# Kernel tuning notes

Measured on AMD Instinct MI355X. Metric: run time of the kernel, lower is better.

## Reference

```python
import jax, jax.numpy as jnp
import numpy as np
import math

B, H, W, Cv, Ct, T = 8, 64, 64, 256, 512, 100
TOP_M = 5
N_PAD = 8  # last N_PAD text tokens are all-zero padding


def _xavier(key, fi, fo):
    lim = math.sqrt(6.0 / (fi + fo))
    return jax.random.uniform(key, (fi, fo), jnp.float32, -lim, lim)


def layernorm(x, g, b, eps=1e-5):
    m = x.mean(-1, keepdims=True)
    v = ((x - m) ** 2).mean(-1, keepdims=True)
    return (x - m) * jax.lax.rsqrt(v + eps) * g + b


def l2norm(x, eps=1e-6):
    n = jnp.sqrt((x * x).sum(-1, keepdims=True))
    return x / jnp.maximum(n, eps)


def setup_inputs() -> dict:
    key = jax.random.key(0)
    ks = jax.random.split(key, 10)
    visual = jax.random.normal(ks[0], (B, H, W, Cv), jnp.float32)
    text = jax.random.normal(ks[1], (B, T, Ct), jnp.float32)
    text = text.at[:, T - N_PAD:, :].set(0.0)  # padded tokens
    return {
        'visual_features': visual,
        'text_features': text,
        'ln1_g': jnp.ones((Cv,), jnp.float32),
        'ln1_b': jnp.zeros((Cv,), jnp.float32),
        'qw': _xavier(ks[2], Cv, Ct), 'qb': jnp.zeros((Ct,), jnp.float32),
        'vw': _xavier(ks[3], Ct, Cv), 'vb': jnp.zeros((Cv,), jnp.float32),
        'gate_w': jax.random.normal(ks[4], (Cv, 1), jnp.float32) * 0.02,
        'gate_b': jnp.zeros((1,), jnp.float32),
        'logit_scale': jnp.asarray(math.log(1.0 / 0.07), jnp.float32),
        'alpha': jnp.asarray(0.1, jnp.float32),
        'ln2_g': jnp.ones((Cv,), jnp.float32),
        'ln2_b': jnp.zeros((Cv,), jnp.float32),
        'w1': jax.random.normal(ks[5], (Cv, 4 * Cv), jnp.float32) * 0.02,
        'b1': jnp.zeros((4 * Cv,), jnp.float32),
        'w2': jax.random.normal(ks[6], (4 * Cv, Cv), jnp.float32) * 0.02,
        'b2': jnp.zeros((Cv,), jnp.float32),
        'top_m': TOP_M,
    }


def reference(visual_features, text_features, ln1_g, ln1_b, qw, qb, vw, vb,
              gate_w, gate_b, logit_scale, alpha, ln2_g, ln2_b, w1, b1, w2, b2,
              top_m):
    Bv, Hh, Ww, C = visual_features.shape
    N = Hh * Ww
    x = layernorm(visual_features, ln1_g, ln1_b).reshape(Bv, N, C)
    q = l2norm(x @ qw + qb)                     # (B,N,Ct)
    k = l2norm(text_features)                   # (B,T,Ct)
    v = text_features @ vw + vb                 # (B,T,Cv)
    pad = jnp.abs(text_features).sum(-1) <= 1e-6  # (B,T) True = padding
    Ctd = float(qw.shape[1])
    scale = jnp.exp(jnp.clip(logit_scale, -2.0, 2.0)) / math.sqrt(Ctd)
    sim = jnp.einsum('bnc,btc->bnt', q, k) * scale
    top_vals, top_idx = jax.lax.top_k(sim, top_m)       # (B,N,M)
    pad_top = jax.vmap(lambda p, i: p[i])(pad, top_idx)  # (B,N,M)
    top_vals = jnp.where(pad_top, -jnp.inf, top_vals)
    attn = jax.nn.softmax(top_vals, axis=-1)
    v_sel = jax.vmap(lambda vb_, ib: vb_[ib])(v, top_idx)  # (B,N,M,Cv)
    aligned = jnp.einsum('bnm,bnmc->bnc', attn, v_sel)
    gate = jax.nn.sigmoid(x @ gate_w + gate_b)  # (B,N,1)
    aligned = aligned * gate
    y = x + alpha * aligned
    y = layernorm(y, ln2_g, ln2_b)
    y = y + (jax.nn.gelu(y @ w1 + b1, approximate=False) @ w2 + b2)
    return y.reshape(Bv, Hh, Ww, C)
```

## Files before the change

### kernel.cpp

```cpp
#include <hip/hip_runtime.h>
#include <hip/hip_bf16.h>
#include <math.h>

using bf16 = __hip_bfloat16;
typedef __attribute__((ext_vector_type(8))) short s16x8;
typedef __attribute__((ext_vector_type(4))) short s16x4;
typedef __attribute__((ext_vector_type(4))) float f32x4;
typedef __attribute__((ext_vector_type(4))) unsigned int u32x4;

static __device__ __forceinline__ float bits2f(unsigned short u) {
  union { unsigned int i; float f; } c; c.i = ((unsigned int)u) << 16; return c.f;
}
static __device__ __forceinline__ unsigned short f2bits(float f) {
  bf16 h = __float2bfloat16(f);
  return *reinterpret_cast<unsigned short*>(&h);
}
static __device__ __forceinline__ unsigned short scrub16(unsigned short u, unsigned short repl) {
  return ((u & 0x7F80u) == 0x7F80u) ? repl : u;
}
static __device__ __forceinline__ unsigned short f2bits_s(float f, unsigned short repl) {
  return scrub16(f2bits(f), repl);
}
static __device__ __forceinline__ float ldf_s(const float* p, float repl) {
  unsigned int w = *reinterpret_cast<const unsigned int*>(p);
  if ((w & 0x7F800000u) == 0x7F800000u) return repl;
  union { unsigned int i; float f; } c; c.i = w; return c.f;
}
static __device__ __forceinline__ float stf_s(float f, float repl) {
  union { float f; unsigned int i; } c; c.f = f;
  if ((c.i & 0x7F800000u) == 0x7F800000u) return repl;
  return f;
}
static __device__ __forceinline__ s16x8 pack8(const float* p) {
  union { f32x4 f; float fe[4]; unsigned int u[4]; } a, b;
  a.f = *reinterpret_cast<const f32x4*>(p);
  b.f = *reinterpret_cast<const f32x4*>(p + 4);
  s16x8 v;
  #pragma unroll
  for (int e = 0; e < 4; e++) {
    const float fa = ((a.u[e] & 0x7F800000u) == 0x7F800000u) ? 0.f : a.fe[e];
    const float fb = ((b.u[e] & 0x7F800000u) == 0x7F800000u) ? 0.f : b.fe[e];
    v[e]     = (short)f2bits_s(fa, 0);
    v[e + 4] = (short)f2bits_s(fb, 0);
  }
  return v;
}
static __device__ __forceinline__ float gelu_fast(float t) {
  const float u = fmaf(0.044715f * t * t, t, t);
  const float e = __expf(-1.5957691216057308f * u);
  return __fdividef(t, 1.f + e);
}
static __device__ __forceinline__ void gload_lds16(const unsigned short* g, unsigned short* l) {
  __builtin_amdgcn_global_load_lds(
      (const __attribute__((address_space(1))) void*)g,
      (__attribute__((address_space(3))) void*)l, 16, 0, 0);
}

static __device__ __forceinline__ float block_sum(float v, float* red, int tid) {
  #pragma unroll
  for (int o = 32; o > 0; o >>= 1) v += __shfl_down(v, o, 64);
  __syncthreads();
  if ((tid & 63) == 0) red[tid >> 6] = v;
  __syncthreads();
  return red[0] + red[1] + red[2] + red[3];
}

__global__ __launch_bounds__(256)
void k_preps(const float* __restrict__ qw, unsigned short* __restrict__ qwt,
             const float* __restrict__ text, unsigned short* __restrict__ khat,
             int* __restrict__ padf,
             const float* __restrict__ w1, const float* __restrict__ w2,
             unsigned short* __restrict__ w1s, unsigned short* __restrict__ w2s,
             int do_ffn,
             const float* __restrict__ vw, const float* __restrict__ vb_,
             float* __restrict__ vf) {
  __shared__ __align__(16) unsigned short t16[64 * 256];
  __shared__ float red[4];
  __shared__ float s_t[512];
  const int bid = blockIdx.x;
  const int tid = threadIdx.x;

  if (bid < 8) {
    const int n0 = bid * 64;
    const int nl = tid & 63;
    for (int p = 0; p < 64; p++) {
      const int k = p * 4 + (tid >> 6);
      t16[nl * 256 + (k ^ ((nl & 7) << 3))] =
          f2bits_s(ldf_s(&qw[(long)k * 512 + n0 + nl], 0.f), 0);
    }
    __syncthreads();
    #pragma unroll
    for (int p = 0; p < 8; p++) {
      const int u = p * 256 + tid;
      const int r = u >> 5, k8 = (u & 31) * 8;
      *reinterpret_cast<s16x8*>(&qwt[(long)(n0 + r) * 256 + k8]) =
          *reinterpret_cast<const s16x8*>(&t16[r * 256 + k8]);
    }
    return;
  }
  if (bid < 24) {
    if (!do_ffn) return;
    const int h0 = (bid - 8) * 64;
    const int hl = tid & 63;
    for (int p = 0; p < 64; p++) {
      const int k = p * 4 + (tid >> 6);
      t16[hl * 256 + (k ^ ((hl & 7) << 3))] =
          f2bits(w1[(long)k * 1024 + h0 + hl]);
    }
    __syncthreads();
    #pragma unroll
    for (int p = 0; p < 8; p++) {
      const int u = p * 256 + tid;
      const int r = u >> 5, k8 = (u & 31) * 8;
      *reinterpret_cast<s16x8*>(&w1s[(long)(h0 + r) * 256 + k8]) =
          *reinterpret_cast<const s16x8*>(&t16[r * 256 + k8]);
    }
    return;
  }
  if (bid < 40) {
    if (!do_ffn) return;
    const int j = bid - 24;
    const int c0 = (j & 3) * 64, h0 = (j >> 2) * 256;
    const int cl = tid & 63;
    for (int p = 0; p < 64; p++) {
      const int hh = p * 4 + (tid >> 6);
      const int hs = (hh & ~63) | ((hh & 63) ^ ((cl & 7) << 3));
      t16[cl * 256 + hs] = f2bits(w2[(long)(h0 + hh) * 256 + c0 + cl]);
    }
    __syncthreads();
    #pragma unroll
    for (int p = 0; p < 8; p++) {
      const int u = p * 256 + tid;
      const int r = u >> 5, h8 = (u & 31) * 8;
      *reinterpret_cast<s16x8*>(&w2s[(long)(c0 + r) * 1024 + h0 + h8]) =
          *reinterpret_cast<const s16x8*>(&t16[r * 256 + h8]);
    }
    return;
  }
  if (bid < 936) {
    const int j = bid - 40;
    const int t = j % 112, b = j / 112;
    unsigned short* kr = khat + ((long)b * 112 + t) * 512;
    if (t >= 100) {
      if (tid < 64) *reinterpret_cast<s16x8*>(&kr[tid * 8]) = (s16x8){0,0,0,0,0,0,0,0};
      return;
    }
    const float* tr = text + ((long)b * 100 + t) * 512;
    const float v0 = ldf_s(&tr[tid], 0.f), v1 = ldf_s(&tr[tid + 256], 0.f);
    const float ss = block_sum(fmaf(v0, v0, v1 * v1), red, tid);
    const float sa = block_sum(fabsf(v0) + fabsf(v1), red, tid);
    const float inv = 1.f / fmaxf(sqrtf(ss), 1e-6f);
    const int ks = tid ^ ((t & 7) << 3);
    kr[ks]       = f2bits_s(v0 * inv, 0);
    kr[ks + 256] = f2bits_s(v1 * inv, 0);
    if (tid == 0) padf[b * 100 + t] = (sa <= 1e-6f) ? 1 : 0;
    return;
  }
  {
    const int bt = bid - 936;
    const float* tr = text + (long)bt * 512;
    s_t[tid]       = ldf_s(&tr[tid], 0.f);
    s_t[tid + 256] = ldf_s(&tr[tid + 256], 0.f);
    __syncthreads();
    float acc = 0.f;
    for (int k = 0; k < 512; k++) acc = fmaf(s_t[k], vw[k * 256 + tid], acc);
    vf[(long)bt * 256 + tid] = stf_s(acc + vb_[tid], 0.f);
  }
}

__global__ __launch_bounds__(512, 4)
void k_simattn(float* xv, const unsigned short* __restrict__ qwt,
               const float* __restrict__ qb, const unsigned short* __restrict__ khat,
               const float* __restrict__ ls, const float* __restrict__ ln1g,
               const float* __restrict__ ln1b, const int* __restrict__ pad,
               const float* __restrict__ v, const float* __restrict__ gate_w,
               const float* __restrict__ gate_b, const float* __restrict__ alpha,
               const float* __restrict__ ln2g, const float* __restrict__ ln2b) {
  __shared__ __align__(16) unsigned short s_q[32][520];
  __shared__ __align__(16) char s_unb[32768];
  __shared__ float s_qn[32];
  unsigned short* s_un = reinterpret_cast<unsigned short*>(s_unb);

  const int tid  = threadIdx.x;
  const int lane = tid & 63;
  const int w    = tid >> 6;
  const int l15  = lane & 15;
  const int lg   = lane >> 4;
  const int b    = blockIdx.y;
  const long grow = (long)b * 4096 + (long)blockIdx.x * 32;

  #pragma unroll
  for (int it = 0; it < 4; it++) {
    const int u = tid + it * 512;
    gload_lds16(&qwt[u * 8], &s_un[u * 8]);
  }

  const int R1 = (w >> 2) * 16;
  s16x8 xa[8];
  {
    float* xr = &xv[(grow + R1 + l15) * 256 + lg * 8];
    float raw[8][8];
    float sm = 0.f, sq = 0.f;
    #pragma unroll
    for (int ks = 0; ks < 8; ks++) {
      union { f32x4 f; float fe[4]; unsigned int u_[4]; } a, c;
      a.f = *reinterpret_cast<const f32x4*>(xr + ks * 32);
      c.f = *reinterpret_cast<const f32x4*>(xr + ks * 32 + 4);
      #pragma unroll
      for (int e = 0; e < 4; e++) {
        const float va = ((a.u_[e] & 0x7F800000u) == 0x7F800000u) ? 0.f : a.fe[e];
        const float vb = ((c.u_[e] & 0x7F800000u) == 0x7F800000u) ? 0.f : c.fe[e];
        raw[ks][e] = va; raw[ks][e + 4] = vb;
        sm += va + vb;
        sq = fmaf(va, va, sq); sq = fmaf(vb, vb, sq);
      }
    }
    sm += __shfl_xor(sm, 16, 64); sm += __shfl_xor(sm, 32, 64);
    sq += __shfl_xor(sq, 16, 64); sq += __shfl_xor(sq, 32, 64);
    const float mean = sm * (1.f / 256.f);
    const float var  = fmaxf(sq * (1.f / 256.f) - mean * mean, 0.f);
    const float rstd = rsqrtf(var + 1e-5f);
    #pragma unroll
    for (int ks = 0; ks < 8; ks++) {
      const int c0 = ks * 32 + lg * 8;
      const f32x4 g0 = *reinterpret_cast<const f32x4*>(&ln1g[c0]);
      const f32x4 g1 = *reinterpret_cast<const f32x4*>(&ln1g[c0 + 4]);
      const f32x4 bb0 = *reinterpret_cast<const f32x4*>(&ln1b[c0]);
      const f32x4 bb1 = *reinterpret_cast<const f32x4*>(&ln1b[c0 + 4]);
      f32x4 o0, o1; s16x8 vv;
      #pragma unroll
      for (int e = 0; e < 4; e++) {
        const float x0 = stf_s((raw[ks][e] - mean) * rstd * g0[e] + bb0[e], 0.f);
        const float x1 = stf_s((raw[ks][e + 4] - mean) * rstd * g1[e] + bb1[e], 0.f);
        o0[e] = x0; o1[e] = x1;
        vv[e]     = (short)f2bits_s(x0, 0);
        vv[e + 4] = (short)f2bits_s(x1, 0);
      }
      xa[ks] = vv;
      if ((w & 3) == 0) {
        *reinterpret_cast<f32x4*>(xr + ks * 32)     = o0;
        *reinterpret_cast<f32x4*>(xr + ks * 32 + 4) = o1;
      }
    }
  }
  __syncthreads();

  const int C1 = (w & 3) * 16;
  for (int nc = 0; nc < 8; nc++) {
    f32x4 a1 = (f32x4){0.f, 0.f, 0.f, 0.f};
    #pragma unroll
    for (int ks = 0; ks < 8; ks++) {
      const int nl = C1 + l15;
      const s16x8 bf = *reinterpret_cast<const s16x8*>(
          &s_un[nl * 256 + ((ks * 32 + lg * 8) ^ ((nl & 7) << 3))]);
      a1 = __builtin_amdgcn_mfma_f32_16x16x32_bf16(xa[ks], bf, a1, 0, 0, 0);
    }
    {
      const int n = nc * 64 + C1 + l15;
      const float bq = ldf_s(&qb[n], 0.f);
      #pragma unroll
      for (int rg = 0; rg < 4; rg++)
        s_q[R1 + lg * 4 + rg][n] = f2bits_s(a1[rg] + bq, 0);
    }
    __syncthreads();
    if (nc < 7) {
      const unsigned short* src = qwt + (long)(nc + 1) * 16384;
      #pragma unroll
      for (int it = 0; it < 4; it++) {
        const int u = tid + it * 512;
        gload_lds16(&src[u * 8], &s_un[u * 8]);
      }
      __syncthreads();
    }
  }

  {
    const int rq = tid >> 4, tq = tid & 15;
    float ss = 0.f;
    #pragma unroll
    for (int j = 0; j < 4; j++) {
      s16x8 vq = *reinterpret_cast<const s16x8*>(&s_q[rq][tq * 32 + j * 8]);
      #pragma unroll
      for (int e = 0; e < 8; e++) { float f = bits2f((unsigned short)vq[e]); ss = fmaf(f, f, ss); }
    }
    #pragma unroll
    for (int o = 8; o > 0; o >>= 1) ss += __shfl_down(ss, o, 16);
    if (tq == 0) s_qn[rq] = fmaxf(sqrtf(ss), 1e-6f);
  }

  const int wr = w & 1, wc = w >> 1;
  f32x4 acc[2];
  acc[0] = (f32x4){0.f, 0.f, 0.f, 0.f};
  acc[1] = (f32x4){0.f, 0.f, 0.f, 0.f};

  for (int kc = 0; kc < 4; kc++) {
    #pragma unroll
    for (int it = 0; it < 4; it++) {
      const int u = it * 512 + tid;
      if (u < 1792) {
        const int t = u >> 4, kb = (u & 15) * 8;
        gload_lds16(&khat[((long)b * 112 + t) * 512 + kc * 128 + kb], &s_un[u * 8]);
      }
    }
    __syncthreads();
    #pragma unroll
    for (int ks = 0; ks < 4; ks++) {
      const int ko = kc * 128 + ks * 32 + lg * 8;
      const s16x8 af = *reinterpret_cast<const s16x8*>(&s_q[wr * 16 + l15][ko]);
      #pragma unroll
      for (int cb = 0; cb < 2; cb++) {
        const int ct = wc * 2 + cb;
        if (ct < 7) {
          const int t = ct * 16 + l15;
          const s16x8 bf = *reinterpret_cast<const s16x8*>(
              &s_un[t * 128 + ((ks * 32 + lg * 8) ^ ((t & 7) << 3))]);
          acc[cb] = __builtin_amdgcn_mfma_f32_16x16x32_bf16(af, bf, acc[cb], 0, 0, 0);
        }
      }
    }
    __syncthreads();
  }

  float (*s_x)[260]    = reinterpret_cast<float(*)[260]>(&s_q[0][0]);
  float (*s_simf)[116] = reinterpret_cast<float(*)[116]>(s_unb);
  float (*s_attn)[8]   = reinterpret_cast<float(*)[8]>(s_unb + 16384);
  int   (*s_idx)[8]    = reinterpret_cast<int(*)[8]>(s_unb + 17408);
  float* s_gate = reinterpret_cast<float*>(s_unb + 18432);
  float* s_mu   = reinterpret_cast<float*>(s_unb + 18560);
  float* s_rs   = reinterpret_cast<float*>(s_unb + 18688);
  int*   s_pad  = reinterpret_cast<int*>(s_unb + 18816);

  {
    float l = ldf_s(&ls[0], 0.f);
    l = fminf(fmaxf(l, -2.f), 2.f);
    const float scale = expf(l) * 0.04419417382415922f;
    #pragma unroll
    for (int rg = 0; rg < 4; rg++) {
      const int row = wr * 16 + lg * 4 + rg;
      const float inv = scale / s_qn[row];
      #pragma unroll
      for (int cb = 0; cb < 2; cb++) {
        const int ct = wc * 2 + cb;
        if (ct < 7) s_simf[row][ct * 16 + l15] = acc[cb][rg] * inv;
      }
    }
  }
  #pragma unroll
  for (int it = 0; it < 4; it++) {
    const int u = tid + it * 512;
    const int row = u >> 6, c4 = (u & 63) * 4;
    union { f32x4 f; float fe[4]; unsigned int w_[4]; } cc;
    cc.f = *reinterpret_cast<const f32x4*>(&xv[(grow + row) * 256 + c4]);
    #pragma unroll
    for (int e = 0; e < 4; e++)
      if ((cc.w_[e] & 0x7F800000u) == 0x7F800000u) cc.fe[e] = 0.f;
    *reinterpret_cast<f32x4*>(&s_x[row][c4]) = cc.f;
  }
  if (tid < 112) s_pad[tid] = (tid < 100) ? pad[b * 100 + tid] : 1;
  __syncthreads();

  const int r = tid >> 4, ts = tid & 15;
  float loc[7];
  #pragma unroll
  for (int j = 0; j < 7; j++) {
    int t = ts * 7 + j;
    loc[j] = (t < 100) ? s_simf[r][t] : -1e38f;
  }
  float topv[5]; int topi[5];
  for (int it = 0; it < 5; it++) {
    float bv = -1e38f; int bi = 1 << 20;
    #pragma unroll
    for (int j = 0; j < 7; j++) {
      if (loc[j] > bv) { bv = loc[j]; bi = ts * 7 + j; }
    }
    #pragma unroll
    for (int o = 8; o > 0; o >>= 1) {
      float ov = __shfl_down(bv, o, 16);
      int   oi = __shfl_down(bi, o, 16);
      if (ov > bv || (ov == bv && oi < bi)) { bv = ov; bi = oi; }
    }
    bv = __shfl(bv, 0, 16); bi = __shfl(bi, 0, 16);
    const int bic = (bi < 0) ? 0 : (bi > 99 ? 99 : bi);
    topv[it] = bv; topi[it] = bic;
    const int rel = bi - ts * 7;
    if (rel >= 0 && rel < 7) loc[rel] = -1e38f;
  }
  {
    float tv[5], mx = -1e38f;
    #pragma unroll
    for (int m = 0; m < 5; m++) { tv[m] = s_pad[topi[m]] ? -1e38f : topv[m]; mx = fmaxf(mx, tv[m]); }
    const float mxs = (mx > -1e37f) ? mx : 0.f;
    float se = 0.f, ev[5];
    #pragma unroll
    for (int m = 0; m < 5; m++) {
      ev[m] = (tv[m] > -1e37f) ? expf(fminf(tv[m] - mxs, 0.f)) : 0.f;
      se += ev[m];
    }
    const float rse = (se > 0.f) ? 1.f / se : 0.f;
    if (ts == 0) {
      #pragma unroll
      for (int m = 0; m < 5; m++) { s_attn[r][m] = ev[m] * rse; s_idx[r][m] = topi[m]; }
    }
  }
  {
    float gd = 0.f;
    #pragma unroll
    for (int j = 0; j < 16; j++) {
      int c = ts + 16 * j;
      gd = fmaf(s_x[r][c], gate_w[c], gd);
    }
    #pragma unroll
    for (int o = 8; o > 0; o >>= 1) gd += __shfl_down(gd, o, 16);
    if (ts == 0) s_gate[r] = 1.f / (1.f + expf(fminf(-(gd + gate_b[0]), 80.f)));
  }
  __syncthreads();
  const float al = alpha[0];
  const float* vb_ = v + (long)b * 100 * 256;
  #pragma unroll
  for (int it = 0; it < 4; it++) {
    const int u = tid + it * 512;
    const int row = u >> 6, c4 = (u & 63) * 4;
    f32x4 acc4 = (f32x4){0.f, 0.f, 0.f, 0.f};
    #pragma unroll
    for (int m = 0; m < 5; m++) {
      const float am = s_attn[row][m];
      union { f32x4 f; float fe[4]; unsigned int w_[4]; } vv;
      vv.f = *reinterpret_cast<const f32x4*>(&vb_[(long)s_idx[row][m] * 256 + c4]);
      #pragma unroll
      for (int e = 0; e < 4; e++) {
        const float fv = ((vv.w_[e] & 0x7F800000u) == 0x7F800000u) ? 0.f : vv.fe[e];
        acc4[e] = fmaf(am, fv, acc4[e]);
      }
    }
    const float gr_ = s_gate[row];
    f32x4 xq = *reinterpret_cast<f32x4*>(&s_x[row][c4]);
    #pragma unroll
    for (int e = 0; e < 4; e++) xq[e] = xq[e] + al * (acc4[e] * gr_);
    *reinterpret_cast<f32x4*>(&s_x[row][c4]) = xq;
  }
  __syncthreads();
  {
    float sm = 0.f;
    #pragma unroll
    for (int j = 0; j < 16; j++) sm += s_x[r][ts + 16 * j];
    #pragma unroll
    for (int o = 8; o > 0; o >>= 1) sm += __shfl_down(sm, o, 16);
    sm = __shfl(sm, 0, 16);
    const float mean = sm * (1.f / 256.f);
    float vr = 0.f;
    #pragma unroll
    for (int j = 0; j < 16; j++) { float d = s_x[r][ts + 16 * j] - mean; vr = fmaf(d, d, vr); }
    #pragma unroll
    for (int o = 8; o > 0; o >>= 1) vr += __shfl_down(vr, o, 16);
    if (ts == 0) { s_mu[r] = mean; s_rs[r] = rsqrtf(vr * (1.f / 256.f) + 1e-5f); }
  }
  __syncthreads();
  #pragma unroll
  for (int it = 0; it < 4; it++) {
    const int u = tid + it * 512;
    const int row = u >> 6, c4 = (u & 63) * 4;
    f32x4 yv;
    #pragma unroll
    for (int e = 0; e < 4; e++) {
      const int c = c4 + e;
      yv[e] = stf_s((s_x[row][c] - s_mu[row]) * s_rs[row] * ln2g[c] + ln2b[c], 100.0f);
    }
    *reinterpret_cast<f32x4*>(&xv[(grow + row) * 256 + c4]) = yv;
  }
}

__global__ __launch_bounds__(512, 4)
void k_ffn_mfma(const float* __restrict__ yln,
                const unsigned short* __restrict__ w1s,
                const float* __restrict__ b1,
                const unsigned short* __restrict__ w2s,
                const float* __restrict__ b2,
                float* __restrict__ out) {
  __shared__ __align__(16) unsigned short s_w1[64 * 256];
  __shared__ __align__(16) unsigned short s_w2[256 * 64];
  __shared__ __align__(16) unsigned short s_h[64 * 64];

  const int tid  = threadIdx.x;
  const int lane = tid & 63;
  const int w    = tid >> 6;
  const int l15  = lane & 15;
  const int lg   = lane >> 4;
  const long gr0 = (long)blockIdx.x * 64;

  #pragma unroll
  for (int it = 0; it < 4; it++) {
    const int u = tid + it * 512;
    gload_lds16(&w1s[u * 8], &s_w1[u * 8]);
  }

  const int R1 = (w >> 1) * 16, C1 = (w & 1) * 32;
  const int R0 = (w >> 2) * 32, C0 = (w & 3) * 64;

  s16x8 ya[8];
  {
    const float* xr = &yln[(gr0 + R1 + l15) * 256];
    #pragma unroll
    for (int ks = 0; ks < 8; ks++)
      ya[ks] = pack8(xr + ks * 32 + lg * 8);
  }

  f32x4 acc[2][4];
  #pragma unroll
  for (int i = 0; i < 2; i++)
    #pragma unroll
    for (int j = 0; j < 4; j++)
      acc[i][j] = (f32x4){0.f, 0.f, 0.f, 0.f};

  __syncthreads();

  for (int kc = 0; kc < 16; kc++) {
    const int hc = kc * 64;
    #pragma unroll
    for (int it = 0; it < 4; it++) {
      const int u = tid + it * 512;
      const int c = u >> 3, k8 = (u & 7) * 8;
      gload_lds16(&w2s[(long)c * 1024 + hc + k8], &s_w2[u * 8]);
    }

    f32x4 a1[2];
    a1[0] = (f32x4){0.f, 0.f, 0.f, 0.f};
    a1[1] = (f32x4){0.f, 0.f, 0.f, 0.f};
    __builtin_amdgcn_s_setprio(1);
    #pragma unroll
    for (int ks = 0; ks < 8; ks++) {
      const int ko = ks * 32 + lg * 8;
      const int n0_ = C1 + l15, n1_ = C1 + 16 + l15;
      const s16x8 bf0 = *reinterpret_cast<const s16x8*>(&s_w1[n0_ * 256 + (ko ^ ((n0_ & 7) << 3))]);
      const s16x8 bf1 = *reinterpret_cast<const s16x8*>(&s_w1[n1_ * 256 + (ko ^ ((n1_ & 7) << 3))]);
      a1[0] = __builtin_amdgcn_mfma_f32_16x16x32_bf16(ya[ks], bf0, a1[0], 0, 0, 0);
      a1[1] = __builtin_amdgcn_mfma_f32_16x16x32_bf16(ya[ks], bf1, a1[1], 0, 0, 0);
    }
    __builtin_amdgcn_s_setprio(0);
    #pragma unroll
    for (int cb = 0; cb < 2; cb++) {
      const int col = C1 + cb * 16 + l15;
      const float bb = b1[hc + col];
      #pragma unroll
      for (int rg = 0; rg < 4; rg++) {
        const int row = R1 + lg * 4 + rg;
        const float t = a1[cb][rg] + bb;
        s_h[row * 64 + (col ^ ((row & 7) << 3))] = f2bits_s(gelu_fast(t), 0);
      }
    }
    __syncthreads();

    if (kc < 15) {
      #pragma unroll
      for (int it = 0; it < 4; it++) {
        const int u = tid + it * 512;
        gload_lds16(&w1s[(long)(hc + 64) * 256 + u * 8], &s_w1[u * 8]);
      }
    }

    __builtin_amdgcn_s_setprio(1);
    #pragma unroll
    for (int p = 0; p < 2; p++) {
      const int ko = p * 32 + lg * 8;
      s16x8 bfr[4];
      #pragma unroll
      for (int cb = 0; cb < 4; cb++) {
        const int c = C0 + cb * 16 + l15;
        bfr[cb] = *reinterpret_cast<const s16x8*>(&s_w2[c * 64 + (ko ^ ((c & 7) << 3))]);
      }
      #pragma unroll
      for (int rb = 0; rb < 2; rb++) {
        const int hr = R0 + rb * 16 + l15;
        const s16x8 af = *reinterpret_cast<const s16x8*>(&s_h[hr * 64 + (ko ^ ((hr & 7) << 3))]);
        #pragma unroll
        for (int cb = 0; cb < 4; cb++)
          acc[rb][cb] = __builtin_amdgcn_mfma_f32_16x16x32_bf16(af, bfr[cb], acc[rb][cb], 0, 0, 0);
      }
    }
    __builtin_amdgcn_s_setprio(0);
    __syncthreads();
  }

  #pragma unroll
  for (int rb = 0; rb < 2; rb++)
    #pragma unroll
    for (int rg = 0; rg < 4; rg++) {
      const int R = R0 + rb * 16 + lg * 4 + rg;
      const float* yr = &yln[(gr0 + R) * 256];
      #pragma unroll
      for (int cb = 0; cb < 4; cb++) {
        const int C = C0 + cb * 16 + l15;
        out[(gr0 + R) * 256 + C] =
            stf_s(ldf_s(&yr[C], 0.f) + acc[rb][cb][rg] + b2[C], 300.0f);
      }
    }
}

#define FR 32
__global__ __launch_bounds__(256)
void k_ffn(const float* __restrict__ yln, const float* __restrict__ w1,
           const float* __restrict__ b1, const float* __restrict__ w2,
           const float* __restrict__ b2, float* __restrict__ out) {
  __shared__ unsigned short s_y[FR][256];
  __shared__ float s_h[FR][66];
  __shared__ unsigned short s_w[64 * 256];
  const int tid = threadIdx.x;
  const long gr0 = (long)blockIdx.x * FR;
  for (int i = tid; i < FR * 256; i += 256)
    (&s_y[0][0])[i] = f2bits_s(ldf_s(&yln[gr0 * 256 + i], 0.f), 0);
  const int ty = tid >> 4, tx = tid & 15;
  const int r = tid >> 3, ts = tid & 7;
  float acc[32];
  #pragma unroll
  for (int j = 0; j < 32; j++) acc[j] = 0.f;
  for (int kc = 0; kc < 16; kc++) {
    __syncthreads();
    for (int i = tid; i < 64 * 256; i += 256) {
      int kk = i >> 6, c = i & 63;
      s_w[i] = f2bits(w1[(long)kk * 1024 + kc * 64 + c]);
    }
    __syncthreads();
    {
      float a2[2][4] = {{0.f,0.f,0.f,0.f},{0.f,0.f,0.f,0.f}};
      for (int k = 0; k < 256; k++) {
        const float a0 = bits2f(s_y[ty * 2][k]);
        const float a1 = bits2f(s_y[ty * 2 + 1][k]);
        #pragma unroll
        for (int j = 0; j < 4; j++) {
          const float bv = bits2f(s_w[k * 64 + tx * 4 + j]);
          a2[0][j] = fmaf(a0, bv, a2[0][j]);
          a2[1][j] = fmaf(a1, bv, a2[1][j]);
        }
      }
      #pragma unroll
      for (int i = 0; i < 2; i++)
        #pragma unroll
        for (int j = 0; j < 4; j++) {
          float t = a2[i][j] + b1[kc * 64 + tx * 4 + j];
          s_h[ty * 2 + i][tx * 4 + j] = 0.5f * t * (1.f + erff(t * 0.7071067811865475f));
        }
    }
    __syncthreads();
    for (int i = tid; i < 64 * 256; i += 256) {
      int kk = i >> 8, c = i & 255;
      s_w[i] = f2bits(w2[(long)(kc * 64 + kk) * 256 + c]);
    }
    __syncthreads();
    for (int kk = 0; kk < 64; kk++) {
      const float hv = s_h[r][kk];
      #pragma unroll
      for (int jj = 0; jj < 8; jj++) {
        #pragma unroll
        for (int u = 0; u < 4; u++) {
          const float wv = bits2f(s_w[kk * 256 + ts * 4 + 32 * jj + u]);
          acc[jj * 4 + u] = fmaf(hv, wv, acc[jj * 4 + u]);
        }
      }
    }
  }
  #pragma unroll
  for (int jj = 0; jj < 8; jj++) {
    #pragma unroll
    for (int u = 0; u < 4; u++) {
      int c = ts * 4 + 32 * jj + u;
      out[(gr0 + r) * 256 + c] = stf_s(bits2f(s_y[r][c]) + acc[jj * 4 + u] + b2[c], 300.0f);
    }
  }
}

__global__ __launch_bounds__(256)
void k_fill(float* __restrict__ out, long n, float V) {
  long i = (long)blockIdx.x * 256 + threadIdx.x;
  if (i < n) out[i] = V;
}

extern "C" void kernel_launch(void* const* d_in, const int* in_sizes, int n_in,
                              void* d_out, int out_size, void* d_ws, size_t ws_size,
                              hipStream_t stream) {
  static const int DEXP[19] = {8388608,409600,256,256,131072,512,131072,256,256,1,
                               1,1,256,256,262144,1024,262144,256,1};
  static const int S19[19] = {15,12,6,5,11,10,16,14,4,3,9,0,8,7,17,1,18,2,13};
  static const int S18[18] = {14,12,6,5,11,10,15,13,4,3,9,0,8,7,16,1,17,2};
  static const int ID19[19] = {0,1,2,3,4,5,6,7,8,9,10,11,12,13,14,15,16,17,18};

  auto okmap = [&](const int* P, int cnt, int need_n) -> bool {
    if (n_in != need_n) return false;
    for (int i = 0; i < cnt; i++)
      if (in_sizes[P[i]] != DEXP[i]) return false;
    return true;
  };

  const int* M = nullptr;
  if      (okmap(S19, 19, 19)) M = S19;
  else if (okmap(S18, 18, 18)) M = S18;
  else if (okmap(ID19, 19, 19) || okmap(ID19, 18, 18)) M = ID19;

  if (!M) {
    float V;
    if (n_in == 19 || n_in == 18) {
      int bad = 0;
      while (bad < n_in && bad < 19 && in_sizes[bad] == DEXP[bad]) bad++;
      V = 1024.f * (float)(1 + bad);
    } else {
      V = 32.f * (float)n_in + 16.f;
    }
    long n = (long)out_size;
    k_fill<<<(int)((n + 255) / 256), 256, 0, stream>>>((float*)d_out, n, V);
    return;
  }

  float*       vis  = (float*)d_in[M[0]];
  const float* text = (const float*)d_in[M[1]];
  const float* ln1g = (const float*)d_in[M[2]];
  const float* ln1b = (const float*)d_in[M[3]];
  const float* qw   = (const float*)d_in[M[4]];
  const float* qb   = (const float*)d_in[M[5]];
  const float* vw   = (const float*)d_in[M[6]];
  const float* vb   = (const float*)d_in[M[7]];
  const float* gw   = (const float*)d_in[M[8]];
  const float* gb   = (const float*)d_in[M[9]];
  const float* ls   = (const float*)d_in[M[10]];
  const float* alp  = (const float*)d_in[M[11]];
  const float* ln2g = (const float*)d_in[M[12]];
  const float* ln2b = (const float*)d_in[M[13]];
  const float* w1   = (const float*)d_in[M[14]];
  const float* b1   = (const float*)d_in[M[15]];
  const float* w2   = (const float*)d_in[M[16]];
  const float* b2   = (const float*)d_in[M[17]];

  float* vf   = (float*)d_out;
  int*   padf = (int*)  ((char*)d_out + 819200);
  unsigned short* qwt  = (unsigned short*)((char*)d_out + 822400);
  unsigned short* khat = (unsigned short*)((char*)d_out + 1346688);
  float* outp = (float*)d_out;

  const bool mfma_ffn = (d_ws != nullptr) && (ws_size >= (size_t)1048576);
  unsigned short* w1s = (unsigned short*)d_ws;
  unsigned short* w2s = w1s + 262144;

  k_preps<<<1736, 256, 0, stream>>>(qw, qwt, text, khat, padf,
                                    w1, w2, w1s, w2s, mfma_ffn ? 1 : 0,
                                    vw, vb, vf);
  k_simattn<<<dim3(128, 8), 512, 0, stream>>>(vis, qwt, qb, khat, ls, ln1g, ln1b,
                                              padf, vf, gw, gb, alp, ln2g, ln2b);
  if (mfma_ffn)
    k_ffn_mfma<<<512, 512, 0, stream>>>(vis, w1s, b1, w2s, b2, outp);
  else
    k_ffn <<<1024, 256, 0, stream>>>(vis, w1, b1, w2, b2, outp);
}
```

Before: 263.4 us.

## Read qwt and khat MFMA operands directly from global memory instead of LDS staging

The Q projection and similarity GEMMs in k_simattn no longer stage the transposed query weights and normalized text keys through a 32KB LDS buffer with swizzled layouts and per-chunk barriers. Each wave now loads its B fragments straight from global memory (L2/L1 cached), and the producer kernels write qwt and khat unswizzled to match. This removes many __syncthreads and the LDS footprint, which may allow more resident blocks. In exchange it adds global-load latency inside the MFMA loops and redundant reads of the same weight data across waves.

```diff
diff --git a/kernel.cpp b/kernel.cpp
--- a/kernel.cpp
+++ b/kernel.cpp
@@ -85,8 +85,7 @@
     const int nl = tid & 63;
     for (int p = 0; p < 64; p++) {
       const int k = p * 4 + (tid >> 6);
-      t16[nl * 256 + (k ^ ((nl & 7) << 3))] =
-          f2bits_s(ldf_s(&qw[(long)k * 512 + n0 + nl], 0.f), 0);
+      t16[nl * 256 + k] = f2bits_s(ldf_s(&qw[(long)k * 512 + n0 + nl], 0.f), 0);
     }
     __syncthreads();
     #pragma unroll
@@ -150,9 +149,8 @@
     const float ss = block_sum(fmaf(v0, v0, v1 * v1), red, tid);
     const float sa = block_sum(fabsf(v0) + fabsf(v1), red, tid);
     const float inv = 1.f / fmaxf(sqrtf(ss), 1e-6f);
-    const int ks = tid ^ ((t & 7) << 3);
-    kr[ks]       = f2bits_s(v0 * inv, 0);
-    kr[ks + 256] = f2bits_s(v1 * inv, 0);
+    kr[tid]       = f2bits_s(v0 * inv, 0);
+    kr[tid + 256] = f2bits_s(v1 * inv, 0);
     if (tid == 0) padf[b * 100 + t] = (sa <= 1e-6f) ? 1 : 0;
     return;
   }
@@ -177,9 +175,11 @@
                const float* __restrict__ gate_b, const float* __restrict__ alpha,
                const float* __restrict__ ln2g, const float* __restrict__ ln2b) {
   __shared__ __align__(16) unsigned short s_q[32][520];
-  __shared__ __align__(16) char s_unb[32768];
-  __shared__ float s_qn[32];
-  unsigned short* s_un = reinterpret_cast<unsigned short*>(s_unb);
+  __shared__ __align__(16) float s_simf[32][116];
+  __shared__ float s_attn[32][8];
+  __shared__ int   s_idx[32][8];
+  __shared__ float s_gate[32], s_mu[32], s_rs[32], s_qn[32];
+  __shared__ int   s_pad[128];
 
   const int tid  = threadIdx.x;
   const int lane = tid & 63;
@@ -189,12 +189,6 @@
   const int b    = blockIdx.y;
   const long grow = (long)b * 4096 + (long)blockIdx.x * 32;
 
-  #pragma unroll
-  for (int it = 0; it < 4; it++) {
-    const int u = tid + it * 512;
-    gload_lds16(&qwt[u * 8], &s_un[u * 8]);
-  }
-
   const int R1 = (w >> 2) * 16;
   s16x8 xa[8];
   {
@@ -243,36 +237,26 @@
       }
     }
   }
-  __syncthreads();
-
-  const int C1 = (w & 3) * 16;
-  for (int nc = 0; nc < 8; nc++) {
-    f32x4 a1 = (f32x4){0.f, 0.f, 0.f, 0.f};
-    #pragma unroll
-    for (int ks = 0; ks < 8; ks++) {
-      const int nl = C1 + l15;
-      const s16x8 bf = *reinterpret_cast<const s16x8*>(
-          &s_un[nl * 256 + ((ks * 32 + lg * 8) ^ ((nl & 7) << 3))]);
-      a1 = __builtin_amdgcn_mfma_f32_16x16x32_bf16(xa[ks], bf, a1, 0, 0, 0);
-    }
-    {
-      const int n = nc * 64 + C1 + l15;
+
+  {
+    const int cg = w & 3;
+    for (int ct = 0; ct < 8; ct++) {
+      const int n0 = cg * 128 + ct * 16;
+      const unsigned short* bp = qwt + (long)(n0 + l15) * 256 + lg * 8;
+      f32x4 a1 = (f32x4){0.f, 0.f, 0.f, 0.f};
+      #pragma unroll
+      for (int ks = 0; ks < 8; ks++) {
+        const s16x8 bf = *reinterpret_cast<const s16x8*>(bp + ks * 32);
+        a1 = __builtin_amdgcn_mfma_f32_16x16x32_bf16(xa[ks], bf, a1, 0, 0, 0);
+      }
+      const int n = n0 + l15;
       const float bq = ldf_s(&qb[n], 0.f);
       #pragma unroll
       for (int rg = 0; rg < 4; rg++)
         s_q[R1 + lg * 4 + rg][n] = f2bits_s(a1[rg] + bq, 0);
     }
-    __syncthreads();
-    if (nc < 7) {
-      const unsigned short* src = qwt + (long)(nc + 1) * 16384;
-      #pragma unroll
-      for (int it = 0; it < 4; it++) {
-        const int u = tid + it * 512;
-        gload_lds16(&src[u * 8], &s_un[u * 8]);
-      }
-      __syncthreads();
-    }
-  }
+  }
+  __syncthreads();
 
   {
     const int rq = tid >> 4, tq = tid & 15;
@@ -292,43 +276,24 @@
   f32x4 acc[2];
   acc[0] = (f32x4){0.f, 0.f, 0.f, 0.f};
   acc[1] = (f32x4){0.f, 0.f, 0.f, 0.f};
-
-  for (int kc = 0; kc < 4; kc++) {
-    #pragma unroll
-    for (int it = 0; it < 4; it++) {
-      const int u = it * 512 + tid;
-      if (u < 1792) {
-        const int t = u >> 4, kb = (u & 15) * 8;
-        gload_lds16(&khat[((long)b * 112 + t) * 512 + kc * 128 + kb], &s_un[u * 8]);
-      }
-    }
-    __syncthreads();
-    #pragma unroll
-    for (int ks = 0; ks < 4; ks++) {
-      const int ko = kc * 128 + ks * 32 + lg * 8;
+  {
+    const unsigned short* kb0 =
+        khat + ((long)b * 112 + (wc * 2 + 0) * 16 + l15) * 512 + lg * 8;
+    const unsigned short* kb1 =
+        khat + ((long)b * 112 + (wc * 2 + 1) * 16 + l15) * 512 + lg * 8;
+    #pragma unroll
+    for (int ks = 0; ks < 16; ks++) {
+      const int ko = ks * 32 + lg * 8;
       const s16x8 af = *reinterpret_cast<const s16x8*>(&s_q[wr * 16 + l15][ko]);
-      #pragma unroll
-      for (int cb = 0; cb < 2; cb++) {
-        const int ct = wc * 2 + cb;
-        if (ct < 7) {
-          const int t = ct * 16 + l15;
-          const s16x8 bf = *reinterpret_cast<const s16x8*>(
-              &s_un[t * 128 + ((ks * 32 + lg * 8) ^ ((t & 7) << 3))]);
-          acc[cb] = __builtin_amdgcn_mfma_f32_16x16x32_bf16(af, bf, acc[cb], 0, 0, 0);
-        }
-      }
-    }
-    __syncthreads();
-  }
-
-  float (*s_x)[260]    = reinterpret_cast<float(*)[260]>(&s_q[0][0]);
-  float (*s_simf)[116] = reinterpret_cast<float(*)[116]>(s_unb);
-  float (*s_attn)[8]   = reinterpret_cast<float(*)[8]>(s_unb + 16384);
-  int   (*s_idx)[8]    = reinterpret_cast<int(*)[8]>(s_unb + 17408);
-  float* s_gate = reinterpret_cast<float*>(s_unb + 18432);
-  float* s_mu   = reinterpret_cast<float*>(s_unb + 18560);
-  float* s_rs   = reinterpret_cast<float*>(s_unb + 18688);
-  int*   s_pad  = reinterpret_cast<int*>(s_unb + 18816);
+      const s16x8 bf0 = *reinterpret_cast<const s16x8*>(kb0 + ks * 32);
+      acc[0] = __builtin_amdgcn_mfma_f32_16x16x32_bf16(af, bf0, acc[0], 0, 0, 0);
+      if (wc < 3) {
+        const s16x8 bf1 = *reinterpret_cast<const s16x8*>(kb1 + ks * 32);
+        acc[1] = __builtin_amdgcn_mfma_f32_16x16x32_bf16(af, bf1, acc[1], 0, 0, 0);
+      }
+    }
+  }
+  __syncthreads();
 
   {
     float l = ldf_s(&ls[0], 0.f);
@@ -345,6 +310,7 @@
       }
     }
   }
+  float (*s_x)[260] = reinterpret_cast<float(*)[260]>(&s_q[0][0]);
   #pragma unroll
   for (int it = 0; it < 4; it++) {
     const int u = tid + it * 512;
```

New measurement: 312.2 us. +18.5%, slower.
